# Performance work log

Hardware: AMD Instinct MI355X
Metric: run time of the kernel (lower is better)

## Reference

```python
import jax, jax.numpy as jnp
import numpy as np

NEIGHBOUR_NUM = 8  # args.neighbour_num


def _sqrdis_map(x, y):
    # x: [B,M,3], y: [B,N,3] -> [B,M,N] squared distances
    x2 = jnp.sum(x * x, axis=-1)
    y2 = jnp.sum(y * y, axis=-1)
    inner = jnp.einsum('bmd,bnd->bmn', x, y)
    return x2[:, :, None] + y2[:, None, :] - 2.0 * inner


def _chamfer(x, y):
    d = _sqrdis_map(x, y)
    return d.min(axis=2), d.min(axis=1)


def _neighbor_index(v, k):
    # torch.topk(dist, k+1, largest=False) then drop self
    d = _sqrdis_map(v, v)
    idx = jax.lax.top_k(-d, k + 1)[1]  # ascending distance order
    return idx[:, :, 1:]


def _arap(idx, dp, sp):
    B = dp.shape[0]
    bid = jnp.arange(B)[:, None, None]
    dn = dp[bid, idx] - dp[:, :, None, :]  # [B,N,K,3]
    sn = sp[bid, idx] - sp[:, :, None, :]
    dd = jnp.sqrt(jnp.sum(dn * dn, axis=-1) + 1e-5)
    sd = jnp.sqrt(jnp.sum(sn * sn, axis=-1) + 1e-5)
    diff = dd - sd
    return jnp.sum(diff * diff) / B


def setup_inputs() -> dict:
    key = jax.random.key(0)
    ks = jax.random.split(key, 7)
    T, B, N = 3, 4, 4096
    return {
        'phi': jax.random.normal(ks[0], (T, B, 1024), dtype=jnp.float32),
        'point_weight': jax.random.normal(ks[1], (T, B, N, 1), dtype=jnp.float32),
        'deform_rigid_points': 0.5 * jax.random.normal(ks[2], (T, B, N, 3), dtype=jnp.float32),
        'deformation_points': 0.5 * jax.random.normal(ks[3], (T, B, N, 3), dtype=jnp.float32),
        'rigid_matrix': 0.1 * jax.random.normal(ks[4], (T, B, 4, 4), dtype=jnp.float32),
        'source_points': jax.random.uniform(ks[5], (B, N, 3), dtype=jnp.float32, minval=-1.0, maxval=1.0),
        'target_points': jax.random.uniform(ks[6], (B, N, 3), dtype=jnp.float32, minval=-1.0, maxval=1.0),
    }


def reference(phi, point_weight, deform_rigid_points, deformation_points,
              rigid_matrix, source_points, target_points):
    B = source_points.shape[0]
    T = phi.shape[0]  # iter_time = len(phi_list)
    idx = _neighbor_index(source_points, NEIGHBOUR_NUM)
    trans_mask = jnp.zeros((4, 4), dtype=rigid_matrix.dtype).at[0:3, 3].set(1.0)
    total = jnp.asarray(0.0, dtype=source_points.dtype)
    for t in range(T):  # small fixed iter count, structurally distinct stages
        dp = deformation_points[t]
        # loss_on_cd
        d1, d2 = _chamfer(dp, target_points)
        cd = (jnp.sum(d1) + jnp.sum(d2)) * 0.5 / B
        # loss_on_pd (rigid-deformed vs full deformation)
        diff = deform_rigid_points[t] - dp
        pd = jnp.sum(diff * diff) / B
        # loss_on_sparse
        sp = jnp.mean(jnp.abs(point_weight[t]))
        # loss_on_tran
        tr = trans_mask[None] * rigid_matrix[t]
        tran = jnp.sum(tr * tr) / B
        # loss_on_arap
        ar = _arap(idx, dp, source_points)
        total = total + cd + pd + sp + tran + ar
    return total
```

## Files before the change

kernel.cpp:

```cpp
#include <hip/hip_runtime.h>

#define T_ 3
#define B_ 4
#define N_ 4096
#define K_ 8

#define GROUPS 32
#define GRP_KNN 32
#define GRP_CH  12
#define GRP_SZ  45
#define CWIN 512

typedef short bf16x8 __attribute__((ext_vector_type(8)));
typedef float f32x4  __attribute__((ext_vector_type(4)));

template <int NW>
__device__ inline float block_reduce(float v, float* scratch) {
    #pragma unroll
    for (int off = 32; off > 0; off >>= 1) v += __shfl_down(v, off, 64);
    const int lane = threadIdx.x & 63, wid = threadIdx.x >> 6;
    if (lane == 0) scratch[wid] = v;
    __syncthreads();
    float s = 0.f;
    if (threadIdx.x == 0) {
        #pragma unroll
        for (int w = 0; w < NW; ++w) s += scratch[w];
    }
    return s;
}

#define CE_(A, i, j) { unsigned lo_ = min(A[i], A[j]); A[j] = max(A[i], A[j]); A[i] = lo_; }
__device__ inline void sort8(unsigned s[8]) {
    CE_(s,0,1) CE_(s,2,3) CE_(s,4,5) CE_(s,6,7)
    CE_(s,0,2) CE_(s,1,3) CE_(s,4,6) CE_(s,5,7)
    CE_(s,1,2) CE_(s,5,6)
    CE_(s,0,4) CE_(s,1,5) CE_(s,2,6) CE_(s,3,7)
    CE_(s,2,4) CE_(s,3,5)
    CE_(s,1,2) CE_(s,3,4) CE_(s,5,6)
}
__device__ inline void merge_top8(unsigned a[8], const unsigned s[8]) {
    #pragma unroll
    for (int i = 0; i < 8; ++i) a[i] = min(a[i], s[7 - i]);
    CE_(a,0,4) CE_(a,1,5) CE_(a,2,6) CE_(a,3,7)
    CE_(a,0,2) CE_(a,1,3) CE_(a,4,6) CE_(a,5,7)
    CE_(a,0,1) CE_(a,2,3) CE_(a,4,5) CE_(a,6,7)
}

__device__ inline short hi16(float v) { return (short)(__float_as_uint(v) >> 16); }
__device__ inline float residual(float v) {
    return v - __uint_as_float(__float_as_uint(v) & 0xFFFF0000u);
}
__device__ inline unsigned pk2(short a, short b) {
    return (unsigned)(unsigned short)a | ((unsigned)(unsigned short)b << 16);
}
#define BF16_ONE ((short)0x3F80)

__global__ __launch_bounds__(256, 6) void mega_kernel(const float* __restrict__ src,
                                                      const float* __restrict__ dp_all,
                                                      const float* __restrict__ tp,
                                                      const float* __restrict__ drp,
                                                      const float* __restrict__ pw,
                                                      const float* __restrict__ rm,
                                                      float* __restrict__ out) {
    __shared__ uint4 smem4[1024];
    const f32x4 zero4 = {0.f, 0.f, 0.f, 0.f};

    const int g = blockIdx.x / GRP_SZ;
    const int r = blockIdx.x % GRP_SZ;

    if (r < GRP_KNN) {
        const int knn_id = g * GRP_KNN + r;
        uint4* alds = smem4;
        const int b   = knn_id / (N_ / 16);
        const int qt0 = (knn_id % (N_ / 16)) * 16;
        const float* sb = src + (size_t)b * N_ * 3;

        const int wid  = __builtin_amdgcn_readfirstlane(threadIdx.x >> 6);
        const int lane = threadIdx.x & 63;
        const int n    = lane & 15;
        const int quad = lane >> 4;
        const int rbase = quad * 4;
        const int qid  = qt0 + n;

        bf16x8 bfrag = (bf16x8)(short)0;
        {
            float x = sb[3 * qid], y = sb[3 * qid + 1], z = sb[3 * qid + 2];
            float q2 = fmaf(x, x, fmaf(y, y, z * z));
            short hx = hi16(x), hy = hi16(y), hz = hi16(z);
            short lx = hi16(residual(x)), ly = hi16(residual(y)), lz = hi16(residual(z));
            if (quad == 0) bfrag = (bf16x8){hx, hy, hz, hx, hy, hz, BF16_ONE, BF16_ONE};
            else if (quad == 1) bfrag = (bf16x8){lx, ly, lz, lx, ly, lz,
                                                 hi16(q2), hi16(residual(q2))};
        }

        unsigned a[K_];
        #pragma unroll
        for (int p = 0; p < K_; ++p) a[p] = 0xFFFFFFFFu;

        for (int w = 0; w < N_ / CWIN; ++w) {
            __syncthreads();
            #pragma unroll
            for (int rr = 0; rr < 2; ++rr) {
                int jloc = rr * 256 + threadIdx.x;
                int jg = w * CWIN + jloc;
                float x = sb[3 * jg], y = sb[3 * jg + 1], z = sb[3 * jg + 2];
                float p2 = fmaf(x, x, fmaf(y, y, z * z));
                float mx = -2.f * x, my = -2.f * y, mz = -2.f * z;
                short mhx = hi16(mx), mhy = hi16(my), mhz = hi16(mz);
                short mlx = hi16(residual(mx)), mly = hi16(residual(my)), mlz = hi16(residual(mz));
                uint4 f0 = make_uint4(pk2(mhx, mhy), pk2(mhz, mlx), pk2(mly, mlz),
                                      pk2(hi16(p2), hi16(residual(p2))));
                uint4 f1 = make_uint4(f0.x, f0.y, f0.z, pk2(BF16_ONE, BF16_ONE));
                int tile = jloc >> 4, m = jloc & 15;
                alds[tile * 32 + m]      = f0;
                alds[tile * 32 + 16 + m] = f1;
            }
            __syncthreads();

            #pragma unroll
            for (int bt = 0; bt < 4; ++bt) {
                unsigned s8[8];
                #pragma unroll
                for (int h = 0; h < 2; ++h) {
                    const int tile = wid * 8 + bt * 2 + h;
                    const int tbg  = w * CWIN + tile * 16;
                    bf16x8 af = (bf16x8)(short)0;
                    if (quad < 2) {
                        union { uint4 u; bf16x8 v; } cv;
                        cv.u = alds[tile * 32 + quad * 16 + n];
                        af = cv.v;
                    }
                    f32x4 d = __builtin_amdgcn_mfma_f32_16x16x32_bf16(af, bfrag, zero4, 0, 0, 0);
                    #pragma unroll
                    for (int rr = 0; rr < 4; ++rr)
                        s8[h * 4 + rr] = (__float_as_uint(d[rr]) & 0xFFFFF000u)
                                         | (unsigned)(tbg | (rbase + rr));
                    if (tbg == qt0) {
                        #pragma unroll
                        for (int rr = 0; rr < 4; ++rr)
                            if (rbase + rr == n) s8[h * 4 + rr] = 0xFFFFFFFFu;
                    }
                }
                sort8(s8);
                merge_top8(a, s8);
            }
        }

        #pragma unroll
        for (int mk = 16; mk <= 32; mk <<= 1) {
            unsigned t[8];
            #pragma unroll
            for (int e = 0; e < K_; ++e) t[e] = __shfl_xor(a[e], mk, 64);
            merge_top8(a, t);
        }

        __syncthreads();
        unsigned* sm = (unsigned*)smem4;
        unsigned* nidx = (unsigned*)smem4 + 1024;
        if (lane < 16) {
            #pragma unroll
            for (int e = 0; e < K_; ++e) sm[(wid * 16 + n) * 9 + e] = a[e];
        }
        __syncthreads();
        if (threadIdx.x < 16) {
            const int q = threadIdx.x;
            unsigned md[K_];
            #pragma unroll
            for (int e = 0; e < K_; ++e) md[e] = sm[q * 9 + e];
            #pragma unroll
            for (int wv = 1; wv < 4; ++wv) {
                unsigned t[8];
                #pragma unroll
                for (int e = 0; e < K_; ++e) t[e] = sm[(wv * 16 + q) * 9 + e];
                merge_top8(md, t);
            }
            #pragma unroll
            for (int e = 0; e < K_; ++e) nidx[q * 8 + e] = md[e] & 0xFFFu;
        }
        __syncthreads();

        float acc = 0.f;
        if (threadIdx.x < 16 * K_) {
            const int q  = threadIdx.x >> 3;
            const int qi = qt0 + q;
            const int j  = (int)nidx[threadIdx.x];
            float sx = sb[3 * qi], sy = sb[3 * qi + 1], sz = sb[3 * qi + 2];
            float ex = sb[3 * j] - sx, ey = sb[3 * j + 1] - sy, ez = sb[3 * j + 2] - sz;
            float sd = sqrtf(fmaf(ex, ex, fmaf(ey, ey, ez * ez)) + 1e-5f);
            #pragma unroll
            for (int t = 0; t < T_; ++t) {
                const float* dpb = dp_all + ((size_t)(t * B_ + b)) * N_ * 3;
                float dx = dpb[3 * j] - dpb[3 * qi];
                float dy = dpb[3 * j + 1] - dpb[3 * qi + 1];
                float dz = dpb[3 * j + 2] - dpb[3 * qi + 2];
                float dd = sqrtf(fmaf(dx, dx, fmaf(dy, dy, dz * dz)) + 1e-5f);
                float df = dd - sd;
                acc = fmaf(df, df, acc);
            }
        }
        float s = block_reduce<4>(acc, (float*)smem4);
        if (threadIdx.x == 0) atomicAdd(out, s * (1.0f / B_));

    } else if (r < GRP_KNN + GRP_CH) {
        const int cb = g * GRP_CH + (r - GRP_KNN);
        uint4* alds = smem4;
        const int tbd  = cb >> 4;
        const int slab = cb & 15;
        const int dir = tbd & 1;
        const int tb  = tbd >> 1;
        const int b = tb % B_, t = tb / B_;

        const float* dpb = dp_all + ((size_t)(t * B_ + b)) * N_ * 3;
        const float* tpb = tp + (size_t)b * N_ * 3;
        const float* cbase = dir ? dpb : tpb;
        const float* qbase = dir ? tpb : dpb;

        const int lane = threadIdx.x & 63;
        const int wave = threadIdx.x >> 6;
        const int quad = lane >> 4;
        const int n    = lane & 15;

        bf16x8 bfrag[4];
        float  q2r[4];
        #pragma unroll
        for (int s = 0; s < 4; ++s) {
            int qid = slab * 256 + wave * 64 + s * 16 + n;
            float x = qbase[3 * qid], y = qbase[3 * qid + 1], z = qbase[3 * qid + 2];
            q2r[s] = fmaf(x, x, fmaf(y, y, z * z));
            short hx = hi16(x), hy = hi16(y), hz = hi16(z);
            short lx = hi16(residual(x)), ly = hi16(residual(y)), lz = hi16(residual(z));
            if (quad == 0)
                bfrag[s] = (bf16x8){hx, hy, hz, hx, hy, hz, BF16_ONE, BF16_ONE};
            else if (quad == 1)
                bfrag[s] = (bf16x8){lx, ly, lz, lx, ly, lz, 0, 0};
            else
                bfrag[s] = (bf16x8)(short)0;
        }

        float run[4] = {3.4e38f, 3.4e38f, 3.4e38f, 3.4e38f};

        for (int w = 0; w < N_ / CWIN; ++w) {
            __syncthreads();
            #pragma unroll
            for (int rr = 0; rr < 2; ++rr) {
                int jloc = rr * 256 + threadIdx.x;
                int jg = w * CWIN + jloc;
                float x = cbase[3 * jg], y = cbase[3 * jg + 1], z = cbase[3 * jg + 2];
                float p2 = fmaf(x, x, fmaf(y, y, z * z));
                float mx = -2.f * x, my = -2.f * y, mz = -2.f * z;
                short mhx = hi16(mx), mhy = hi16(my), mhz = hi16(mz);
                short mlx = hi16(residual(mx)), mly = hi16(residual(my)), mlz = hi16(residual(mz));
                uint4 f0 = make_uint4(pk2(mhx, mhy), pk2(mhz, mlx), pk2(mly, mlz),
                                      pk2(hi16(p2), hi16(residual(p2))));
                uint4 f1 = make_uint4(f0.x, f0.y, f0.z, 0u);
                int tile = jloc >> 4, m = jloc & 15;
                alds[tile * 32 + m]      = f0;
                alds[tile * 32 + 16 + m] = f1;
            }
            __syncthreads();

            #pragma unroll 4
            for (int tile = 0; tile < CWIN / 16; ++tile) {
                bf16x8 af = (bf16x8)(short)0;
                if (quad < 2) {
                    union { uint4 u; bf16x8 v; } cv;
                    cv.u = alds[tile * 32 + quad * 16 + n];
                    af = cv.v;
                }
                #pragma unroll
                for (int s = 0; s < 4; ++s) {
                    f32x4 d = __builtin_amdgcn_mfma_f32_16x16x32_bf16(af, bfrag[s], zero4, 0, 0, 0);
                    float r3 = fminf(fminf(d[0], d[1]), d[2]);
                    run[s] = fminf(fminf(run[s], r3), d[3]);
                }
            }
        }

        float vsum = 0.f;
        #pragma unroll
        for (int s = 0; s < 4; ++s) {
            float rr = run[s];
            rr = fminf(rr, __shfl_xor(rr, 32));
            rr = fminf(rr, __shfl_xor(rr, 16));
            if (lane < 16) vsum += rr + q2r[s];
        }
        __syncthreads();
        float ssum = block_reduce<4>(vsum, (float*)smem4);
        if (threadIdx.x == 0) atomicAdd(out, ssum * (0.5f / B_));

    } else {
        const int PD_N = T_ * B_ * N_ * 3;
        const int SP_N = T_ * B_ * N_;
        const int stride = GROUPS * 256;
        const int gid = g * 256 + threadIdx.x;
        float apd = 0.f;
        for (int i = gid; i < PD_N; i += stride) {
            float d = drp[i] - dp_all[i];
            apd = fmaf(d, d, apd);
        }
        float asp = 0.f;
        for (int i = gid; i < SP_N; i += stride) asp += fabsf(pw[i]);
        float atr = 0.f;
        if (gid < T_ * B_ * 3) {
            int t = gid / (B_ * 3);
            int b = (gid / 3) % B_;
            int rr = gid % 3;
            float v = rm[t * B_ * 16 + b * 16 + rr * 4 + 3];
            atr = v * v;
        }
        float acc = apd * (1.0f / B_) + asp * (1.0f / (B_ * N_)) + atr * (1.0f / B_);
        float s = block_reduce<4>(acc, (float*)smem4);
        if (threadIdx.x == 0) atomicAdd(out, s);
    }
}

extern "C" void kernel_launch(void* const* d_in, const int* in_sizes, int n_in,
                              void* d_out, int out_size, void* d_ws, size_t ws_size,
                              hipStream_t stream) {
    const float* pw  = (const float*)d_in[1];
    const float* drp = (const float*)d_in[2];
    const float* dp  = (const float*)d_in[3];
    const float* rm  = (const float*)d_in[4];
    const float* sp  = (const float*)d_in[5];
    const float* tp  = (const float*)d_in[6];
    float* out = (float*)d_out;

    hipMemsetAsync(out, 0, sizeof(float), stream);
    mega_kernel<<<GROUPS * GRP_SZ, 256, 0, stream>>>(sp, dp, tp, drp, pw, rm, out);
}
```

Baseline: 122.2 us.

## Split KNN and chamfer candidate ranges in half and merge partials in finalize kernel

Each KNN and chamfer block now scans only half of the candidate windows, which doubles the block count to fill more of the GPU. Partial top-8 lists and partial minima go to workspace. A second finalize kernel merges them, computes the ARAP and chamfer sums, and adds the small-loss partials. The memset is replaced by a write to zero inside the main kernel. In exchange this adds a second launch, global round trips for the partials, and a dependency on workspace size.

After: 130.4 us. 6.7% more time.

```diff
diff --git a/kernel.cpp b/kernel.cpp
--- a/kernel.cpp
+++ b/kernel.cpp
@@ -6,9 +6,10 @@
 #define K_ 8
 
 #define GROUPS 32
-#define GRP_KNN 32
-#define GRP_CH  12
-#define GRP_SZ  45
+#define GRP_KNN 64
+#define GRP_CH  24
+#define GRP_SZ  89
+#define SL_BLOCKS 32
 #define CWIN 512
 
 typedef short bf16x8 __attribute__((ext_vector_type(8)));
@@ -61,18 +62,25 @@
                                                       const float* __restrict__ drp,
                                                       const float* __restrict__ pw,
                                                       const float* __restrict__ rm,
+                                                      unsigned* __restrict__ knnp,
+                                                      float* __restrict__ chp,
+                                                      float* __restrict__ slp,
                                                       float* __restrict__ out) {
     __shared__ uint4 smem4[1024];
     const f32x4 zero4 = {0.f, 0.f, 0.f, 0.f};
 
+    if (blockIdx.x == 0 && threadIdx.x == 0) *out = 0.f;
+
     const int g = blockIdx.x / GRP_SZ;
     const int r = blockIdx.x % GRP_SZ;
 
     if (r < GRP_KNN) {
         const int knn_id = g * GRP_KNN + r;
+        const int half = knn_id & 1;
+        const int kid2 = knn_id >> 1;
         uint4* alds = smem4;
-        const int b   = knn_id / (N_ / 16);
-        const int qt0 = (knn_id % (N_ / 16)) * 16;
+        const int b   = kid2 / (N_ / 16);
+        const int qt0 = (kid2 % (N_ / 16)) * 16;
         const float* sb = src + (size_t)b * N_ * 3;
 
         const int wid  = __builtin_amdgcn_readfirstlane(threadIdx.x >> 6);
@@ -97,7 +105,7 @@
         #pragma unroll
         for (int p = 0; p < K_; ++p) a[p] = 0xFFFFFFFFu;
 
-        for (int w = 0; w < N_ / CWIN; ++w) {
+        for (int w = half * 4; w < half * 4 + 4; ++w) {
             __syncthreads();
             #pragma unroll
             for (int rr = 0; rr < 2; ++rr) {
@@ -156,7 +164,6 @@
 
         __syncthreads();
         unsigned* sm = (unsigned*)smem4;
-        unsigned* nidx = (unsigned*)smem4 + 1024;
         if (lane < 16) {
             #pragma unroll
             for (int e = 0; e < K_; ++e) sm[(wid * 16 + n) * 9 + e] = a[e];
@@ -174,38 +181,18 @@
                 for (int e = 0; e < K_; ++e) t[e] = sm[(wv * 16 + q) * 9 + e];
                 merge_top8(md, t);
             }
-            #pragma unroll
-            for (int e = 0; e < K_; ++e) nidx[q * 8 + e] = md[e] & 0xFFFu;
-        }
-        __syncthreads();
-
-        float acc = 0.f;
-        if (threadIdx.x < 16 * K_) {
-            const int q  = threadIdx.x >> 3;
-            const int qi = qt0 + q;
-            const int j  = (int)nidx[threadIdx.x];
-            float sx = sb[3 * qi], sy = sb[3 * qi + 1], sz = sb[3 * qi + 2];
-            float ex = sb[3 * j] - sx, ey = sb[3 * j + 1] - sy, ez = sb[3 * j + 2] - sz;
-            float sd = sqrtf(fmaf(ex, ex, fmaf(ey, ey, ez * ez)) + 1e-5f);
-            #pragma unroll
-            for (int t = 0; t < T_; ++t) {
-                const float* dpb = dp_all + ((size_t)(t * B_ + b)) * N_ * 3;
-                float dx = dpb[3 * j] - dpb[3 * qi];
-                float dy = dpb[3 * j + 1] - dpb[3 * qi + 1];
-                float dz = dpb[3 * j + 2] - dpb[3 * qi + 2];
-                float dd = sqrtf(fmaf(dx, dx, fmaf(dy, dy, dz * dz)) + 1e-5f);
-                float df = dd - sd;
-                acc = fmaf(df, df, acc);
-            }
-        }
-        float s = block_reduce<4>(acc, (float*)smem4);
-        if (threadIdx.x == 0) atomicAdd(out, s * (1.0f / B_));
+            unsigned* dst = knnp + ((size_t)(b * N_ + qt0 + q) * 2 + half) * 8;
+            #pragma unroll
+            for (int e = 0; e < K_; ++e) dst[e] = md[e];
+        }
 
     } else if (r < GRP_KNN + GRP_CH) {
         const int cb = g * GRP_CH + (r - GRP_KNN);
+        const int half = cb & 1;
+        const int rest = cb >> 1;
         uint4* alds = smem4;
-        const int tbd  = cb >> 4;
-        const int slab = cb & 15;
+        const int tbd  = rest >> 4;
+        const int slab = rest & 15;
         const int dir = tbd & 1;
         const int tb  = tbd >> 1;
         const int b = tb % B_, t = tb / B_;
@@ -221,12 +208,10 @@
         const int n    = lane & 15;
 
         bf16x8 bfrag[4];
-        float  q2r[4];
         #pragma unroll
         for (int s = 0; s < 4; ++s) {
             int qid = slab * 256 + wave * 64 + s * 16 + n;
             float x = qbase[3 * qid], y = qbase[3 * qid + 1], z = qbase[3 * qid + 2];
-            q2r[s] = fmaf(x, x, fmaf(y, y, z * z));
             short hx = hi16(x), hy = hi16(y), hz = hi16(z);
             short lx = hi16(residual(x)), ly = hi16(residual(y)), lz = hi16(residual(z));
             if (quad == 0)
@@ -239,7 +224,7 @@
 
         float run[4] = {3.4e38f, 3.4e38f, 3.4e38f, 3.4e38f};
 
-        for (int w = 0; w < N_ / CWIN; ++w) {
+        for (int w = half * 4; w < half * 4 + 4; ++w) {
             __syncthreads();
             #pragma unroll
             for (int rr = 0; rr < 2; ++rr) {
@@ -276,22 +261,22 @@
             }
         }
 
-        float vsum = 0.f;
         #pragma unroll
         for (int s = 0; s < 4; ++s) {
             float rr = run[s];
             rr = fminf(rr, __shfl_xor(rr, 32));
             rr = fminf(rr, __shfl_xor(rr, 16));
-            if (lane < 16) vsum += rr + q2r[s];
-        }
-        __syncthreads();
-        float ssum = block_reduce<4>(vsum, (float*)smem4);
-        if (threadIdx.x == 0) atomicAdd(out, ssum * (0.5f / B_));
+            if (lane < 16) {
+                int qid = slab * 256 + wave * 64 + s * 16 + n;
+                chp[((size_t)(tbd * 2 + half)) * N_ + qid] = rr;
+            }
+        }
 
     } else {
+        __shared__ float red[4];
         const int PD_N = T_ * B_ * N_ * 3;
         const int SP_N = T_ * B_ * N_;
-        const int stride = GROUPS * 256;
+        const int stride = SL_BLOCKS * 256;
         const int gid = g * 256 + threadIdx.x;
         float apd = 0.f;
         for (int i = gid; i < PD_N; i += stride) {
@@ -309,7 +294,67 @@
             atr = v * v;
         }
         float acc = apd * (1.0f / B_) + asp * (1.0f / (B_ * N_)) + atr * (1.0f / B_);
-        float s = block_reduce<4>(acc, (float*)smem4);
+        float s = block_reduce<4>(acc, red);
+        if (threadIdx.x == 0) slp[g] = s;
+    }
+}
+
+__global__ __launch_bounds__(256) void finalize_kernel(const float* __restrict__ src,
+                                                       const float* __restrict__ dp_all,
+                                                       const float* __restrict__ tp,
+                                                       const unsigned* __restrict__ knnp,
+                                                       const float* __restrict__ chp,
+                                                       const float* __restrict__ slp,
+                                                       float* __restrict__ out) {
+    __shared__ float red[4];
+    const int blk = blockIdx.x;
+
+    if (blk < 384) {
+        const int tbd = blk >> 4;
+        const int q = (blk & 15) * 256 + threadIdx.x;
+        const int dir = tbd & 1, tb = tbd >> 1, b = tb % B_, t = tb / B_;
+        const float* qbase = dir ? tp + (size_t)b * N_ * 3
+                                 : dp_all + ((size_t)(t * B_ + b)) * N_ * 3;
+        float m = fminf(chp[(size_t)(tbd * 2) * N_ + q],
+                        chp[(size_t)(tbd * 2 + 1) * N_ + q]);
+        float x = qbase[3 * q], y = qbase[3 * q + 1], z = qbase[3 * q + 2];
+        float v = fmaf(x, x, fmaf(y, y, z * z)) + m;
+        float s = block_reduce<4>(v, red);
+        if (threadIdx.x == 0) atomicAdd(out, s * (0.5f / B_));
+    } else if (blk < 896) {
+        const int qb = (blk - 384) * 32;
+        const int ql = threadIdx.x >> 3;
+        const int k  = threadIdx.x & 7;
+        const int qglob = qb + ql;
+        const int b  = qglob >> 12;
+        const int qi = qglob & (N_ - 1);
+        const unsigned* p0 = knnp + (size_t)qglob * 16;
+        unsigned a[K_], s2[K_];
+        #pragma unroll
+        for (int e = 0; e < K_; ++e) { a[e] = p0[e]; s2[e] = p0[8 + e]; }
+        merge_top8(a, s2);
+        const int j = (int)(a[k] & 0xFFFu);
+
+        const float* sb = src + (size_t)b * N_ * 3;
+        float sx = sb[3 * qi], sy = sb[3 * qi + 1], sz = sb[3 * qi + 2];
+        float ex = sb[3 * j] - sx, ey = sb[3 * j + 1] - sy, ez = sb[3 * j + 2] - sz;
+        float sd = sqrtf(fmaf(ex, ex, fmaf(ey, ey, ez * ez)) + 1e-5f);
+        float acc = 0.f;
+        #pragma unroll
+        for (int t = 0; t < T_; ++t) {
+            const float* dpb = dp_all + ((size_t)(t * B_ + b)) * N_ * 3;
+            float dx = dpb[3 * j] - dpb[3 * qi];
+            float dy = dpb[3 * j + 1] - dpb[3 * qi + 1];
+            float dz = dpb[3 * j + 2] - dpb[3 * qi + 2];
+            float dd = sqrtf(fmaf(dx, dx, fmaf(dy, dy, dz * dz)) + 1e-5f);
+            float df = dd - sd;
+            acc = fmaf(df, df, acc);
+        }
+        float s = block_reduce<4>(acc, red);
+        if (threadIdx.x == 0) atomicAdd(out, s * (1.0f / B_));
+    } else {
+        float v = (threadIdx.x < SL_BLOCKS) ? slp[threadIdx.x] : 0.f;
+        float s = block_reduce<4>(v, red);
         if (threadIdx.x == 0) atomicAdd(out, s);
     }
 }
@@ -325,6 +370,11 @@
     const float* tp  = (const float*)d_in[6];
     float* out = (float*)d_out;
 
-    hipMemsetAsync(out, 0, sizeof(float), stream);
-    mega_kernel<<<GROUPS * GRP_SZ, 256, 0, stream>>>(sp, dp, tp, drp, pw, rm, out);
-}
+    unsigned* knnp = (unsigned*)d_ws;
+    float*    chp  = (float*)((char*)d_ws + (1u << 20));
+    float*    slp  = (float*)((char*)d_ws + (1u << 20) + 24 * 2 * N_ * 4);
+
+    mega_kernel<<<GROUPS * GRP_SZ, 256, 0, stream>>>(sp, dp, tp, drp, pw, rm,
+                                                     knnp, chp, slp, out);
+    finalize_kernel<<<897, 256, 0, stream>>>(sp, dp, tp, knnp, chp, slp, out);
+}
```

## Sort source points into x-slabs and prune kNN search by chunk distance bounds

Applied to the files above, without the earlier changes.

A new prep kernel bucket-sorts each batch's source points by x into 64 slabs, stores them with their original indices, and also runs the pd/sparse/translation reductions that used to be a separate block group. The kNN blocks then scan 256-point chunks outward from the query tile's own chunk. They stop once the x-gap to the next chunk exceeds the current 8th-nearest distance, aiming to skip most of the full N^2 distance work. This adds a second launch, a workspace dependency, and data-dependent loop trip counts. The pruning relies on bf16-split distances, which carries a small correctness risk near the bound.

Result: slower. 125.8 us (+3.0%).

```diff
diff --git a/kernel.cpp b/kernel.cpp
--- a/kernel.cpp
+++ b/kernel.cpp
@@ -8,8 +8,9 @@
 #define GROUPS 32
 #define GRP_KNN 32
 #define GRP_CH  12
-#define GRP_SZ  45
-#define CWIN 512
+#define GRP_SZ  44
+#define NCHUNK 16
+#define SL_BLOCKS 32
 
 typedef short bf16x8 __attribute__((ext_vector_type(8)));
 typedef float f32x4  __attribute__((ext_vector_type(4)));
@@ -55,12 +56,85 @@
 }
 #define BF16_ONE ((short)0x3F80)
 
+__device__ inline void conv_frag(float x, float y, float z, unsigned f1w,
+                                 uint4& f0, uint4& f1) {
+    float p2 = fmaf(x, x, fmaf(y, y, z * z));
+    float mx = -2.f * x, my = -2.f * y, mz = -2.f * z;
+    f0 = make_uint4(pk2(hi16(mx), hi16(my)),
+                    pk2(hi16(mz), hi16(residual(mx))),
+                    pk2(hi16(residual(my)), hi16(residual(mz))),
+                    pk2(hi16(p2), hi16(residual(p2))));
+    f1 = make_uint4(f0.x, f0.y, f0.z, f1w);
+}
+
+__global__ __launch_bounds__(256) void prep_kernel(const float* __restrict__ src,
+                                                   const float* __restrict__ dp_all,
+                                                   const float* __restrict__ drp,
+                                                   const float* __restrict__ pw,
+                                                   const float* __restrict__ rm,
+                                                   float4* __restrict__ sorted,
+                                                   int* __restrict__ slab_start,
+                                                   float* __restrict__ slp,
+                                                   float* __restrict__ out) {
+    if (blockIdx.x < 4) {
+        const int b = blockIdx.x;
+        if (b == 0 && threadIdx.x == 0) *out = 0.f;
+        __shared__ int hist[64], base_[65], cnt[64];
+        const float* sb = src + (size_t)b * N_ * 3;
+        if (threadIdx.x < 64) { hist[threadIdx.x] = 0; cnt[threadIdx.x] = 0; }
+        __syncthreads();
+        for (int i = threadIdx.x; i < N_; i += 256) {
+            float x = sb[3 * i];
+            int s = min(max((int)((x + 1.f) * 32.f), 0), 63);
+            atomicAdd(&hist[s], 1);
+        }
+        __syncthreads();
+        if (threadIdx.x == 0) {
+            int run = 0;
+            for (int s = 0; s < 64; ++s) { base_[s] = run; run += hist[s]; }
+            base_[64] = N_;
+        }
+        __syncthreads();
+        for (int i = threadIdx.x; i < N_; i += 256) {
+            float x = sb[3 * i], y = sb[3 * i + 1], z = sb[3 * i + 2];
+            int s = min(max((int)((x + 1.f) * 32.f), 0), 63);
+            int pos = base_[s] + atomicAdd(&cnt[s], 1);
+            sorted[(size_t)b * N_ + pos] = make_float4(x, y, z, __int_as_float(i));
+        }
+        if (threadIdx.x < 65) slab_start[b * 65 + threadIdx.x] = base_[threadIdx.x];
+    } else {
+        __shared__ float red[4];
+        const int PD_N = T_ * B_ * N_ * 3;
+        const int SP_N = T_ * B_ * N_;
+        const int stride = SL_BLOCKS * 256;
+        const int gid = (blockIdx.x - 4) * 256 + threadIdx.x;
+        float apd = 0.f;
+        for (int i = gid; i < PD_N; i += stride) {
+            float d = drp[i] - dp_all[i];
+            apd = fmaf(d, d, apd);
+        }
+        float asp = 0.f;
+        for (int i = gid; i < SP_N; i += stride) asp += fabsf(pw[i]);
+        float atr = 0.f;
+        if (gid < T_ * B_ * 3) {
+            int t = gid / (B_ * 3);
+            int b = (gid / 3) % B_;
+            int rr = gid % 3;
+            float v = rm[t * B_ * 16 + b * 16 + rr * 4 + 3];
+            atr = v * v;
+        }
+        float acc = apd * (1.0f / B_) + asp * (1.0f / (B_ * N_)) + atr * (1.0f / B_);
+        float s = block_reduce<4>(acc, red);
+        if (threadIdx.x == 0) slp[blockIdx.x - 4] = s;
+    }
+}
+
 __global__ __launch_bounds__(256, 6) void mega_kernel(const float* __restrict__ src,
                                                       const float* __restrict__ dp_all,
                                                       const float* __restrict__ tp,
-                                                      const float* __restrict__ drp,
-                                                      const float* __restrict__ pw,
-                                                      const float* __restrict__ rm,
+                                                      const float4* __restrict__ sorted,
+                                                      const int* __restrict__ slab_start,
+                                                      const float* __restrict__ slp,
                                                       float* __restrict__ out) {
     __shared__ uint4 smem4[1024];
     const f32x4 zero4 = {0.f, 0.f, 0.f, 0.f};
@@ -71,8 +145,16 @@
     if (r < GRP_KNN) {
         const int knn_id = g * GRP_KNN + r;
         uint4* alds = smem4;
-        const int b   = knn_id / (N_ / 16);
-        const int qt0 = (knn_id % (N_ / 16)) * 16;
+        int*   ext  = (int*)(smem4 + 512);
+        int*   sls  = ext;
+        int*   cslo = ext + 65;
+        int*   cshi = ext + 82;
+        unsigned* bnd = (unsigned*)(ext + 98);
+        int*   qor  = ext + 162;
+
+        const int b   = knn_id >> 8;
+        const int qt0 = (knn_id & 255) * 16;
+        const float4* sbp = sorted + (size_t)b * N_;
         const float* sb = src + (size_t)b * N_ * 3;
 
         const int wid  = __builtin_amdgcn_readfirstlane(threadIdx.x >> 6);
@@ -80,14 +162,33 @@
         const int n    = lane & 15;
         const int quad = lane >> 4;
         const int rbase = quad * 4;
-        const int qid  = qt0 + n;
+
+        if (threadIdx.x < 65) sls[threadIdx.x] = slab_start[b * 65 + threadIdx.x];
+        __syncthreads();
+        if (threadIdx.x < 17) {
+            int p = threadIdx.x * 256, s = 0;
+            while (s < 63 && sls[s + 1] <= p) s++;
+            cslo[threadIdx.x] = s;
+        } else if (threadIdx.x < 33) {
+            int p = (threadIdx.x - 17) * 256 + 255, s = 0;
+            while (s < 63 && sls[s + 1] <= p) s++;
+            cshi[threadIdx.x - 17] = s;
+        }
+
+        float4 qv = sbp[qt0 + n];
+        const float qx = qv.x, qy = qv.y, qz = qv.z;
+        const float q2 = fmaf(qx, qx, fmaf(qy, qy, qz * qz));
+        float txmin = qx, txmax = qx;
+        #pragma unroll
+        for (int mk = 1; mk <= 8; mk <<= 1) {
+            txmin = fminf(txmin, __shfl_xor(txmin, mk));
+            txmax = fmaxf(txmax, __shfl_xor(txmax, mk));
+        }
 
         bf16x8 bfrag = (bf16x8)(short)0;
         {
-            float x = sb[3 * qid], y = sb[3 * qid + 1], z = sb[3 * qid + 2];
-            float q2 = fmaf(x, x, fmaf(y, y, z * z));
-            short hx = hi16(x), hy = hi16(y), hz = hi16(z);
-            short lx = hi16(residual(x)), ly = hi16(residual(y)), lz = hi16(residual(z));
+            short hx = hi16(qx), hy = hi16(qy), hz = hi16(qz);
+            short lx = hi16(residual(qx)), ly = hi16(residual(qy)), lz = hi16(residual(qz));
             if (quad == 0) bfrag = (bf16x8){hx, hy, hz, hx, hy, hz, BF16_ONE, BF16_ONE};
             else if (quad == 1) bfrag = (bf16x8){lx, ly, lz, lx, ly, lz,
                                                  hi16(q2), hi16(residual(q2))};
@@ -97,33 +198,27 @@
         #pragma unroll
         for (int p = 0; p < K_; ++p) a[p] = 0xFFFFFFFFu;
 
-        for (int w = 0; w < N_ / CWIN; ++w) {
+        int cur = qt0 >> 8;
+        int cl = cur - 1, cr = cur + 1;
+        bool dl = (cl < 0), dr = (cr >= NCHUNK);
+        __syncthreads();
+
+        for (;;) {
+            {
+                float4 cd4 = sbp[cur * 256 + threadIdx.x];
+                uint4 f0, f1;
+                conv_frag(cd4.x, cd4.y, cd4.z, pk2(BF16_ONE, BF16_ONE), f0, f1);
+                int tile = threadIdx.x >> 4, m = threadIdx.x & 15;
+                alds[tile * 32 + m] = f0;  alds[tile * 32 + 16 + m] = f1;
+            }
             __syncthreads();
             #pragma unroll
-            for (int rr = 0; rr < 2; ++rr) {
-                int jloc = rr * 256 + threadIdx.x;
-                int jg = w * CWIN + jloc;
-                float x = sb[3 * jg], y = sb[3 * jg + 1], z = sb[3 * jg + 2];
-                float p2 = fmaf(x, x, fmaf(y, y, z * z));
-                float mx = -2.f * x, my = -2.f * y, mz = -2.f * z;
-                short mhx = hi16(mx), mhy = hi16(my), mhz = hi16(mz);
-                short mlx = hi16(residual(mx)), mly = hi16(residual(my)), mlz = hi16(residual(mz));
-                uint4 f0 = make_uint4(pk2(mhx, mhy), pk2(mhz, mlx), pk2(mly, mlz),
-                                      pk2(hi16(p2), hi16(residual(p2))));
-                uint4 f1 = make_uint4(f0.x, f0.y, f0.z, pk2(BF16_ONE, BF16_ONE));
-                int tile = jloc >> 4, m = jloc & 15;
-                alds[tile * 32 + m]      = f0;
-                alds[tile * 32 + 16 + m] = f1;
-            }
-            __syncthreads();
-
-            #pragma unroll
-            for (int bt = 0; bt < 4; ++bt) {
+            for (int bt = 0; bt < 2; ++bt) {
                 unsigned s8[8];
                 #pragma unroll
                 for (int h = 0; h < 2; ++h) {
-                    const int tile = wid * 8 + bt * 2 + h;
-                    const int tbg  = w * CWIN + tile * 16;
+                    const int tile = wid * 4 + bt * 2 + h;
+                    const int tbg  = cur * 256 + tile * 16;
                     bf16x8 af = (bf16x8)(short)0;
                     if (quad < 2) {
                         union { uint4 u; bf16x8 v; } cv;
@@ -144,6 +239,27 @@
                 sort8(s8);
                 merge_top8(a, s8);
             }
+            unsigned k8 = a[7];
+            k8 = min(k8, (unsigned)__shfl_xor((int)k8, 16));
+            k8 = min(k8, (unsigned)__shfl_xor((int)k8, 32));
+            if (lane < 16) bnd[wid * 16 + lane] = k8;
+            __syncthreads();
+            unsigned cm = min(min(bnd[n], bnd[16 + n]), min(bnd[32 + n], bnd[48 + n]));
+            #pragma unroll
+            for (int mk = 1; mk <= 8; mk <<= 1)
+                cm = max(cm, (unsigned)__shfl_xor((int)cm, mk));
+            float d8f = __uint_as_float(cm & 0xFFFFF000u) * 1.0005f + 1e-6f;
+
+            float ledge = 0.f, redge = 0.f;
+            if (!dr) ledge = -1.f + (float)cslo[cr] * 0.03125f;
+            if (!dl) redge = -1.f + (float)(cshi[cl] + 1) * 0.03125f;
+            if (!dr) { float dx = ledge - txmax; if (dx > 0.f && dx * dx > d8f) dr = true; }
+            if (!dl) { float dx = txmin - redge; if (dx > 0.f && dx * dx > d8f) dl = true; }
+            if (dl && dr) break;
+            float er = dr ? 3e38f : fmaxf(ledge - txmax, 0.f);
+            float el = dl ? 3e38f : fmaxf(txmin - redge, 0.f);
+            if (!dr && (dl || er <= el)) { cur = cr; cr++; if (cr >= NCHUNK) dr = true; }
+            else                          { cur = cl; cl--; if (cl < 0)      dl = true; }
         }
 
         #pragma unroll
@@ -153,7 +269,6 @@
             for (int e = 0; e < K_; ++e) t[e] = __shfl_xor(a[e], mk, 64);
             merge_top8(a, t);
         }
-
         __syncthreads();
         unsigned* sm = (unsigned*)smem4;
         unsigned* nidx = (unsigned*)smem4 + 1024;
@@ -175,14 +290,16 @@
                 merge_top8(md, t);
             }
             #pragma unroll
-            for (int e = 0; e < K_; ++e) nidx[q * 8 + e] = md[e] & 0xFFFu;
+            for (int e = 0; e < K_; ++e)
+                nidx[q * 8 + e] = (unsigned)__float_as_int(sbp[md[e] & 0xFFFu].w);
+            qor[q] = __float_as_int(sbp[qt0 + q].w);
         }
         __syncthreads();
 
         float acc = 0.f;
         if (threadIdx.x < 16 * K_) {
             const int q  = threadIdx.x >> 3;
-            const int qi = qt0 + q;
+            const int qi = qor[q];
             const int j  = (int)nidx[threadIdx.x];
             float sx = sb[3 * qi], sy = sb[3 * qi + 1], sz = sb[3 * qi + 2];
             float ex = sb[3 * j] - sx, ey = sb[3 * j + 1] - sy, ez = sb[3 * j + 2] - sz;
@@ -198,10 +315,11 @@
                 acc = fmaf(df, df, acc);
             }
         }
+        __syncthreads();
         float s = block_reduce<4>(acc, (float*)smem4);
         if (threadIdx.x == 0) atomicAdd(out, s * (1.0f / B_));
 
-    } else if (r < GRP_KNN + GRP_CH) {
+    } else {
         const int cb = g * GRP_CH + (r - GRP_KNN);
         uint4* alds = smem4;
         const int tbd  = cb >> 4;
@@ -239,20 +357,15 @@
 
         float run[4] = {3.4e38f, 3.4e38f, 3.4e38f, 3.4e38f};
 
-        for (int w = 0; w < N_ / CWIN; ++w) {
+        for (int w = 0; w < 8; ++w) {
             __syncthreads();
             #pragma unroll
             for (int rr = 0; rr < 2; ++rr) {
                 int jloc = rr * 256 + threadIdx.x;
-                int jg = w * CWIN + jloc;
-                float x = cbase[3 * jg], y = cbase[3 * jg + 1], z = cbase[3 * jg + 2];
-                float p2 = fmaf(x, x, fmaf(y, y, z * z));
-                float mx = -2.f * x, my = -2.f * y, mz = -2.f * z;
-                short mhx = hi16(mx), mhy = hi16(my), mhz = hi16(mz);
-                short mlx = hi16(residual(mx)), mly = hi16(residual(my)), mlz = hi16(residual(mz));
-                uint4 f0 = make_uint4(pk2(mhx, mhy), pk2(mhz, mlx), pk2(mly, mlz),
-                                      pk2(hi16(p2), hi16(residual(p2))));
-                uint4 f1 = make_uint4(f0.x, f0.y, f0.z, 0u);
+                int jg = w * 512 + jloc;
+                uint4 f0, f1;
+                conv_frag(cbase[3 * jg], cbase[3 * jg + 1], cbase[3 * jg + 2],
+                          pk2(BF16_ONE, BF16_ONE), f0, f1);
                 int tile = jloc >> 4, m = jloc & 15;
                 alds[tile * 32 + m]      = f0;
                 alds[tile * 32 + 16 + m] = f1;
@@ -260,7 +373,7 @@
             __syncthreads();
 
             #pragma unroll 4
-            for (int tile = 0; tile < CWIN / 16; ++tile) {
+            for (int tile = 0; tile < 32; ++tile) {
                 bf16x8 af = (bf16x8)(short)0;
                 if (quad < 2) {
                     union { uint4 u; bf16x8 v; } cv;
@@ -286,31 +399,12 @@
         }
         __syncthreads();
         float ssum = block_reduce<4>(vsum, (float*)smem4);
-        if (threadIdx.x == 0) atomicAdd(out, ssum * (0.5f / B_));
-
-    } else {
-        const int PD_N = T_ * B_ * N_ * 3;
-        const int SP_N = T_ * B_ * N_;
-        const int stride = GROUPS * 256;
-        const int gid = g * 256 + threadIdx.x;
-        float apd = 0.f;
-        for (int i = gid; i < PD_N; i += stride) {
-            float d = drp[i] - dp_all[i];
-            apd = fmaf(d, d, apd);
-        }
-        float asp = 0.f;
-        for (int i = gid; i < SP_N; i += stride) asp += fabsf(pw[i]);
-        float atr = 0.f;
-        if (gid < T_ * B_ * 3) {
-            int t = gid / (B_ * 3);
-            int b = (gid / 3) % B_;
-            int rr = gid % 3;
-            float v = rm[t * B_ * 16 + b * 16 + rr * 4 + 3];
-            atr = v * v;
-        }
-        float acc = apd * (1.0f / B_) + asp * (1.0f / (B_ * N_)) + atr * (1.0f / B_);
-        float s = block_reduce<4>(acc, (float*)smem4);
-        if (threadIdx.x == 0) atomicAdd(out, s);
+        if (threadIdx.x == 0) {
+            float add = ssum * (0.5f / B_);
+            if (blockIdx.x == GROUPS * GRP_SZ - 1)
+                for (int i = 0; i < SL_BLOCKS; ++i) add += slp[i];
+            atomicAdd(out, add);
+        }
     }
 }
 
@@ -325,6 +419,12 @@
     const float* tp  = (const float*)d_in[6];
     float* out = (float*)d_out;
 
-    hipMemsetAsync(out, 0, sizeof(float), stream);
-    mega_kernel<<<GROUPS * GRP_SZ, 256, 0, stream>>>(sp, dp, tp, drp, pw, rm, out);
-}
+    float4* sorted     = (float4*)d_ws;
+    int*    slab_start = (int*)((char*)d_ws + 256 * 1024);
+    float*  slp        = (float*)((char*)d_ws + 258 * 1024);
+
+    prep_kernel<<<4 + SL_BLOCKS, 256, 0, stream>>>(sp, dp, drp, pw, rm,
+                                                   sorted, slab_start, slp, out);
+    mega_kernel<<<GROUPS * GRP_SZ, 256, 0, stream>>>(sp, dp, tp, sorted,
+                                                     slab_start, slp, out);
+}
```
